# Performance work log

Measured on AMD Instinct MI355X. Metric: run time of the kernel, lower is better.

The kernel has to match this reference:

```python
import jax, jax.numpy as jnp
import numpy as np

D_MODEL = 1024
D_STATE = 8          # max(8, 16 // 2)
D_CONV = 4
D_INNER = int(1.5 * D_MODEL)   # expand = max(1.5, 2*0.75)
DT_RANK = (D_MODEL + 15) // 16 # 64
D_FF = 2 * D_MODEL
B, L = 2, 2048


def layer_norm(x, g, b, eps=1e-5):
    mu = jnp.mean(x, -1, keepdims=True)
    var = jnp.var(x, -1, keepdims=True)
    return (x - mu) * jax.lax.rsqrt(var + eps) * g + b


def setup_inputs() -> dict:
    key = jax.random.key(0)
    ks = jax.random.split(key, 12)
    def n(k, shape, scale=0.02):
        return jax.random.normal(k, shape, dtype=jnp.float32) * scale
    return {
        'x': jax.random.normal(ks[0], (B, L, D_MODEL), dtype=jnp.float32),
        'ln1_g': jnp.ones((D_MODEL,), jnp.float32),
        'ln1_b': jnp.zeros((D_MODEL,), jnp.float32),
        'ln2_g': jnp.ones((D_MODEL,), jnp.float32),
        'ln2_b': jnp.zeros((D_MODEL,), jnp.float32),
        'in_proj_w': n(ks[1], (2 * D_INNER, D_MODEL)),
        'conv_w': n(ks[2], (D_INNER, 1, D_CONV), 0.1),
        'conv_b': jnp.zeros((D_INNER,), jnp.float32),
        'x_proj_w': n(ks[3], (DT_RANK + 2 * D_STATE, D_INNER)),
        'dt_proj_w': n(ks[4], (D_INNER, DT_RANK), 0.1),
        'dt_proj_b': n(ks[5], (D_INNER,), 0.1),
        'A_log': jnp.log(jnp.broadcast_to(jnp.arange(1, D_STATE + 1, dtype=jnp.float32), (D_INNER, D_STATE))),
        'D': jnp.ones((D_INNER,), jnp.float32),
        'out_proj_w': n(ks[6], (D_MODEL, D_INNER)),
        'ffn_w1': n(ks[7], (D_FF, D_MODEL)),
        'ffn_b1': jnp.zeros((D_FF,), jnp.float32),
        'ffn_w2': n(ks[8], (D_MODEL, D_FF)),
        'ffn_b2': jnp.zeros((D_MODEL,), jnp.float32),
    }


def mamba(x, in_proj_w, conv_w, conv_b, x_proj_w, dt_proj_w, dt_proj_b, A_log, Dp, out_proj_w):
    # in_proj -> (x, z)
    xz = x @ in_proj_w.T                       # (B, L, 2*d_inner)
    xi, z = jnp.split(xz, 2, axis=-1)
    # depthwise causal conv over seq, kernel 4
    xc = jnp.transpose(xi, (0, 2, 1))          # (B, d_inner, L)
    xc = jax.lax.conv_general_dilated(
        xc, conv_w, window_strides=(1,), padding=[(D_CONV - 1, 0)],
        dimension_numbers=('NCH', 'OIH', 'NCH'), feature_group_count=D_INNER)
    xc = xc + conv_b[None, :, None]
    u = jax.nn.silu(jnp.transpose(xc, (0, 2, 1)))  # (B, L, d_inner)
    # x_proj -> dt, B, C
    x_dbl = u @ x_proj_w.T
    dt = x_dbl[..., :DT_RANK]
    Bm = x_dbl[..., DT_RANK:DT_RANK + D_STATE]
    Cm = x_dbl[..., DT_RANK + D_STATE:]
    delta = jax.nn.softplus(dt @ dt_proj_w.T + dt_proj_b)  # (B, L, d_inner)
    A = -jnp.exp(A_log)                                    # (d_inner, d_state)
    dA = jnp.exp(jnp.einsum('bld,dn->bldn', delta, A))     # (B, L, d_inner, d_state)
    dBu = jnp.einsum('bld,bln,bld->bldn', delta, Bm, u)
    # selective scan over time
    def step(h, inputs):
        dA_t, dBu_t, C_t = inputs
        h = dA_t * h + dBu_t                   # (B, d_inner, d_state)
        y = jnp.einsum('bdn,bn->bd', h, C_t)
        return h, y
    h0 = jnp.zeros((x.shape[0], D_INNER, D_STATE), x.dtype)
    _, ys = jax.lax.scan(step, h0, (jnp.moveaxis(dA, 1, 0), jnp.moveaxis(dBu, 1, 0), jnp.moveaxis(Cm, 1, 0)))
    y = jnp.moveaxis(ys, 0, 1) + u * Dp        # skip connection D*u
    y = y * jax.nn.silu(z)                     # gate
    return y @ out_proj_w.T


def reference(x, ln1_g, ln1_b, ln2_g, ln2_b, in_proj_w, conv_w, conv_b, x_proj_w,
              dt_proj_w, dt_proj_b, A_log, D, out_proj_w, ffn_w1, ffn_b1, ffn_w2, ffn_b2):
    residual = x
    xp = layer_norm(x, ln1_g, ln1_b)
    x = mamba(xp, in_proj_w, conv_w, conv_b, x_proj_w, dt_proj_w, dt_proj_b, A_log, D, out_proj_w) + residual
    xn = layer_norm(x, ln2_g, ln2_b)
    h = jax.nn.gelu(xn @ ffn_w1.T + ffn_b1, approximate=False)  # dropout is identity in eval
    return x + (h @ ffn_w2.T + ffn_b2)
```

## Files before the change

### kernel.cpp

```cpp
#include <hip/hip_runtime.h>
#include <math.h>

#define D_MODEL 1024
#define D_STATE 8
#define D_CONV  4
#define D_INNER 1536
#define DT_RANK 64
#define D_FF    2048
#define BATCH   2
#define SEQ     2048
#define NROWS   (BATCH*SEQ)
#define NC      32
#define LC      (SEQ/NC)
#define XPAD    128

typedef short bf16x8 __attribute__((ext_vector_type(8)));
typedef unsigned short u16x8 __attribute__((ext_vector_type(8)));
typedef float f32x4  __attribute__((ext_vector_type(4)));

__device__ inline unsigned short f2bf(float x) {
    union { float f; unsigned u; } v; v.f = x;
    unsigned r = v.u + 0x7fffu + ((v.u >> 16) & 1u);
    return (unsigned short)(r >> 16);
}
__device__ inline float bf2f(unsigned short h) {
    union { unsigned u; float f; } v; v.u = ((unsigned)h) << 16;
    return v.f;
}
__device__ inline float softplus_f(float x) {
    return (x > 20.0f) ? x : log1pf(__expf(x));
}
__device__ inline float gelu_f(float x) {
    return 0.5f * x * (1.0f + erff(x * 0.70710678118654752f));
}
__device__ inline float silu_f(float x) {
    return x / (1.0f + __expf(-x));
}
__device__ inline void gload16(const unsigned short* g, unsigned short* l) {
    typedef unsigned int u32;
    __builtin_amdgcn_global_load_lds(
        (const __attribute__((address_space(1))) u32*)g,
        (__attribute__((address_space(3))) u32*)l, 16, 0, 0);
}

#define PHASE_SYNC_PRE()  do { __builtin_amdgcn_s_barrier(); \
                               asm volatile("s_waitcnt lgkmcnt(0)" ::: "memory"); } while (0)
#define PHASE_SYNC_POST() do { __builtin_amdgcn_s_barrier(); } while (0)

__global__ __launch_bounds__(256) void prep_kernel(
    const float* __restrict__ s0, unsigned short* __restrict__ d0,
    const float* __restrict__ s1, unsigned short* __restrict__ d1,
    const float* __restrict__ s2, unsigned short* __restrict__ d2,
    const float* __restrict__ s3, unsigned short* __restrict__ d3,
    const float* __restrict__ s4, unsigned short* __restrict__ d4,
    const float* __restrict__ xpw, unsigned short* __restrict__ xpd,
    const float* __restrict__ x, const float* __restrict__ g1,
    const float* __restrict__ b1, unsigned short* __restrict__ xout) {
    int b = blockIdx.x;
    if (b < 4400) {
        const float* s; unsigned short* d; int base;
        if      (b < 1536) { s = s0; d = d0; base = b * 2048; }
        else if (b < 1584) { s = s1; d = d1; base = (b - 1536) * 2048; }
        else if (b < 2352) { s = s2; d = d2; base = (b - 1584) * 2048; }
        else if (b < 3376) { s = s3; d = d3; base = (b - 2352) * 2048; }
        else               { s = s4; d = d4; base = (b - 3376) * 2048; }
        int i = base + threadIdx.x * 8;
        float4 v0 = *(const float4*)(s + i);
        float4 v1 = *(const float4*)(s + i + 4);
        ushort4 a, c;
        a.x = f2bf(v0.x); a.y = f2bf(v0.y); a.z = f2bf(v0.z); a.w = f2bf(v0.w);
        c.x = f2bf(v1.x); c.y = f2bf(v1.y); c.z = f2bf(v1.z); c.w = f2bf(v1.w);
        *(ushort4*)(d + i)     = a;
        *(ushort4*)(d + i + 4) = c;
    } else if (b < 4528) {
        int row = b - 4400;
        for (int c = threadIdx.x; c < D_INNER; c += 256)
            xpd[row * D_INNER + c] = (row < 80) ? f2bf(xpw[row * D_INNER + c]) : (unsigned short)0;
    } else {
        __shared__ float sbuf[4];
        int row = b - 4528;
        int t = threadIdx.x;
        float4 v = ((const float4*)(x + (size_t)row * D_MODEL))[t];
        float s = v.x + v.y + v.z + v.w;
        for (int o = 32; o; o >>= 1) s += __shfl_down(s, o, 64);
        if ((t & 63) == 0) sbuf[t >> 6] = s;
        __syncthreads();
        float mu = (sbuf[0] + sbuf[1] + sbuf[2] + sbuf[3]) * (1.0f / D_MODEL);
        __syncthreads();
        float e0 = v.x - mu, e1 = v.y - mu, e2 = v.z - mu, e3 = v.w - mu;
        float q = e0*e0 + e1*e1 + e2*e2 + e3*e3;
        for (int o = 32; o; o >>= 1) q += __shfl_down(q, o, 64);
        if ((t & 63) == 0) sbuf[t >> 6] = q;
        __syncthreads();
        float var = (sbuf[0] + sbuf[1] + sbuf[2] + sbuf[3]) * (1.0f / D_MODEL);
        float rs = rsqrtf(var + 1e-5f);
        float4 gv = ((const float4*)g1)[t];
        float4 bv = ((const float4*)b1)[t];
        ushort4 st;
        st.x = f2bf(e0 * rs * gv.x + bv.x);
        st.y = f2bf(e1 * rs * gv.y + bv.y);
        st.z = f2bf(e2 * rs * gv.z + bv.z);
        st.w = f2bf(e3 * rs * gv.w + bv.w);
        ((ushort4*)(xout + (size_t)row * D_MODEL))[t] = st;
    }
}

#define EPI_F32        0
#define EPI_F32_BF16   1
#define EPI_SOFTPLUS   2
#define EPI_RESID      3
#define EPI_GELU_BF16  4
#define EPI_BIAS_RESID 5
#define EPI_BF16       6
#define EPI_SOFTPLUS_BF16 7
#define EPI_PBF16      9

template<int WN, int EPI, int SPLITK>
__global__ __launch_bounds__(512, 2) void gemm8p(
    const unsigned short* __restrict__ A, int lda,
    const unsigned short* __restrict__ Bm, int ldb, int K,
    float* __restrict__ Cf, unsigned short* __restrict__ Cb, int ldc,
    const float* __restrict__ bias,
    const float* __restrict__ resid, int ldr) {
    constexpr int WM = 8 / WN;
    constexpr int BN = WN * 64;
    constexpr int RW = 256 / WM;
    constexpr int CW = 64;
    constexpr int MI = RW / 16;
    constexpr int NI = CW / 16;
    constexpr int MIH = MI / 2, NIH = NI / 2;
    constexpr int ABYTES = 256 * 128;
    constexpr int BBYTES = BN * 128;
    constexpr int BOFF = 2 * ABYTES;
    __shared__ unsigned short lds[(2 * ABYTES + 2 * BBYTES) / 2];

    const int t = threadIdx.x, l = t & 63, w = t >> 6;
    const int wr = w / WN, wc = w % WN;

    const int nx = gridDim.x;
    const int nwg = nx * gridDim.y;
    int bid = blockIdx.y * nx + blockIdx.x;
    int q = nwg >> 3;
    int swz = (bid & 7) * q + (bid >> 3);
    const int m0 = (swz / nx) * 256, n0 = (swz % nx) * BN;
    const int kbase = (SPLITK > 1) ? blockIdx.z * K : 0;

    const int sr = l >> 3;
    const int sj = ((l & 7) * 16) ^ ((l >> 3) << 4);
    const int row_l = w * 8;
    const int row_c = (w >> 2) * 64 + (w & 3) * 8;

    auto STG = [&](int bufbyte, int rowbase, const unsigned short* G, int ldg, int gbase, int kt) {
        unsigned short* dst = (unsigned short*)((char*)lds + bufbyte + rowbase * 128);
        const unsigned short* src = G + (size_t)(gbase + rowbase + sr) * ldg + kbase + kt * 64 + (sj >> 1);
        gload16(src, dst);
    };
    auto S_Ah0 = [&](int b, int kt) {
        if (WN == 4) { STG(b * ABYTES, row_l, A, lda, m0, kt);       STG(b * ABYTES, 128 + row_l, A, lda, m0, kt); }
        else         { STG(b * ABYTES, row_c, A, lda, m0, kt);       STG(b * ABYTES, 128 + row_c, A, lda, m0, kt); }
    };
    auto S_Ah1 = [&](int b, int kt) {
        if (WN == 4) { STG(b * ABYTES, 64 + row_l, A, lda, m0, kt);  STG(b * ABYTES, 192 + row_l, A, lda, m0, kt); }
        else         { STG(b * ABYTES, 32 + row_c, A, lda, m0, kt);  STG(b * ABYTES, 160 + row_c, A, lda, m0, kt); }
    };
    auto S_Bc0 = [&](int b, int kt) {
        if (WN == 4) { STG(BOFF + b * BBYTES, row_c, Bm, ldb, n0, kt); STG(BOFF + b * BBYTES, 128 + row_c, Bm, ldb, n0, kt); }
        else         { STG(BOFF + b * BBYTES, row_c, Bm, ldb, n0, kt); }
    };
    auto S_Bc1 = [&](int b, int kt) {
        if (WN == 4) { STG(BOFF + b * BBYTES, 32 + row_c, Bm, ldb, n0, kt); STG(BOFF + b * BBYTES, 160 + row_c, Bm, ldb, n0, kt); }
        else         { STG(BOFF + b * BBYTES, 32 + row_c, Bm, ldb, n0, kt); }
    };

    auto LD = [&](int bytebase, int row, int kb) -> bf16x8 {
        int o = bytebase + row * 128 + (kb ^ ((row & 7) << 4));
        return *(const bf16x8*)((const char*)lds + o);
    };

    f32x4 acc[MI][NI] = {};
    bf16x8 af[MIH][2], b0v[NIH][2], b1v[NIH][2];

    auto LDA_set = [&](int buf, int qr, auto& dst) {
        #pragma unroll
        for (int mi = 0; mi < MIH; mi++)
            #pragma unroll
            for (int ks = 0; ks < 2; ks++)
                dst[mi][ks] = LD(buf * ABYTES, wr * RW + qr * (RW / 2) + mi * 16 + (l & 15),
                                 ks * 64 + (l >> 4) * 16);
    };
    auto LDB_set = [&](int buf, int qc, auto& dst) {
        #pragma unroll
        for (int ni2 = 0; ni2 < NIH; ni2++)
            #pragma unroll
            for (int ks = 0; ks < 2; ks++)
                dst[ni2][ks] = LD(BOFF + buf * BBYTES, wc * CW + qc * 32 + ni2 * 16 + (l & 15),
                                  ks * 64 + (l >> 4) * 16);
    };
    auto MFMA_Q = [&](int qr, int qc, auto& a_, auto& b_) {
        __builtin_amdgcn_s_setprio(1);
        #pragma unroll
        for (int mi = 0; mi < MIH; mi++)
            #pragma unroll
            for (int ni2 = 0; ni2 < NIH; ni2++)
                #pragma unroll
                for (int ks = 0; ks < 2; ks++)
                    acc[qr * MIH + mi][qc * NIH + ni2] =
                        __builtin_amdgcn_mfma_f32_16x16x32_bf16(a_[mi][ks], b_[ni2][ks],
                                                                acc[qr * MIH + mi][qc * NIH + ni2], 0, 0, 0);
        __builtin_amdgcn_s_setprio(0);
    };
    auto VMW = [&](bool last) {
        if (last)            asm volatile("s_waitcnt vmcnt(0)" ::: "memory");
        else if (WN == 4)    asm volatile("s_waitcnt vmcnt(6)" ::: "memory");
        else                 asm volatile("s_waitcnt vmcnt(5)" ::: "memory");
    };

    const int ni_ = K >> 7;

    S_Ah0(0, 0); S_Ah1(0, 0); S_Bc0(0, 0); S_Bc1(0, 0);
    S_Ah0(1, 1); S_Ah1(1, 1); S_Bc0(1, 1); S_Bc1(1, 1);
    if (WN == 4) asm volatile("s_waitcnt vmcnt(8)" ::: "memory");
    else         asm volatile("s_waitcnt vmcnt(6)" ::: "memory");
    __builtin_amdgcn_s_barrier();

    for (int i = 0; i < ni_; i++) {
        const bool last = (i == ni_ - 1);
        const int t2 = 2 * i + 2, t3 = 2 * i + 3;
        LDA_set(0, 0, af); LDB_set(0, 0, b0v);
        if (i) S_Bc0(1, 2 * i + 1);
        PHASE_SYNC_PRE(); MFMA_Q(0, 0, af, b0v); PHASE_SYNC_POST();
        LDB_set(0, 1, b1v);
        if (!last) S_Ah0(0, t2);
        PHASE_SYNC_PRE(); MFMA_Q(0, 1, af, b1v); PHASE_SYNC_POST();
        LDA_set(0, 1, af);
        PHASE_SYNC_PRE(); MFMA_Q(1, 1, af, b1v); PHASE_SYNC_POST();
        LDB_set(0, 0, b0v);
        if (!last) { S_Ah1(0, t2); S_Bc1(0, t2); }
        VMW(last);
        PHASE_SYNC_PRE(); MFMA_Q(1, 0, af, b0v); PHASE_SYNC_POST();
        LDA_set(1, 0, af); LDB_set(1, 0, b0v);
        if (!last) S_Bc0(0, t2);
        PHASE_SYNC_PRE(); MFMA_Q(0, 0, af, b0v); PHASE_SYNC_POST();
        LDB_set(1, 1, b1v);
        if (!last) S_Ah0(1, t3);
        PHASE_SYNC_PRE(); MFMA_Q(0, 1, af, b1v); PHASE_SYNC_POST();
        LDA_set(1, 1, af);
        PHASE_SYNC_PRE(); MFMA_Q(1, 1, af, b1v); PHASE_SYNC_POST();
        LDB_set(1, 0, b0v);
        if (!last) { S_Ah1(1, t3); S_Bc1(1, t3); }
        VMW(last);
        PHASE_SYNC_PRE(); MFMA_Q(1, 0, af, b0v); PHASE_SYNC_POST();
    }

    float* Cfp = Cf;
    unsigned short* Cbp = Cb;
    if (SPLITK > 1) {
        Cfp += (size_t)blockIdx.z * NROWS * ldc;
        Cbp += (size_t)blockIdx.z * NROWS * ldc;
    }
    #pragma unroll
    for (int ni2 = 0; ni2 < NI; ni2++) {
        int col = n0 + wc * CW + ni2 * 16 + (l & 15);
        float bv = 0.0f;
        if (EPI == EPI_SOFTPLUS || EPI == EPI_GELU_BF16 || EPI == EPI_BIAS_RESID) bv = bias[col];
        #pragma unroll
        for (int mi = 0; mi < MI; mi++) {
            #pragma unroll
            for (int j = 0; j < 4; j++) {
                int row = m0 + wr * RW + mi * 16 + (l >> 4) * 4 + j;
                float v = acc[mi][ni2][j];
                if (EPI == EPI_SOFTPLUS)        v = softplus_f(v + bv);
                else if (EPI == EPI_GELU_BF16)  v = gelu_f(v + bv);
                else if (EPI == EPI_RESID)      v = v + resid[(size_t)row * ldr + col];
                else if (EPI == EPI_BIAS_RESID) v = v + bv + resid[(size_t)row * ldr + col];
                if (EPI == EPI_GELU_BF16 || EPI == EPI_BF16 || EPI == EPI_PBF16) {
                    Cbp[(size_t)row * ldc + col] = f2bf(v);
                } else {
                    Cfp[(size_t)row * ldc + col] = v;
                    if (EPI == EPI_F32_BF16) Cbp[(size_t)row * ldc + col] = f2bf(v);
                }
            }
        }
    }
}

__global__ __launch_bounds__(256) void sk2_ln(const unsigned short* __restrict__ p,
                                              const float* __restrict__ resid,
                                              const float* __restrict__ g,
                                              const float* __restrict__ b,
                                              float* __restrict__ x2,
                                              unsigned short* __restrict__ xn) {
    __shared__ float sbuf[4];
    int row = blockIdx.x;
    int t = threadIdx.x;
    const size_t seg = (size_t)NROWS * D_MODEL;
    size_t base = (size_t)row * D_MODEL + t * 4;
    ushort4 a = *(const ushort4*)(p + base);
    ushort4 bb = *(const ushort4*)(p + base + seg);
    float4 r = *(const float4*)(resid + base);
    float4 v;
    v.x = bf2f(a.x) + bf2f(bb.x) + r.x;
    v.y = bf2f(a.y) + bf2f(bb.y) + r.y;
    v.z = bf2f(a.z) + bf2f(bb.z) + r.z;
    v.w = bf2f(a.w) + bf2f(bb.w) + r.w;
    *(float4*)(x2 + base) = v;
    float s = v.x + v.y + v.z + v.w;
    for (int o = 32; o; o >>= 1) s += __shfl_down(s, o, 64);
    if ((t & 63) == 0) sbuf[t >> 6] = s;
    __syncthreads();
    float mu = (sbuf[0] + sbuf[1] + sbuf[2] + sbuf[3]) * (1.0f / D_MODEL);
    __syncthreads();
    float d0 = v.x - mu, d1 = v.y - mu, d2 = v.z - mu, d3 = v.w - mu;
    float qq = d0*d0 + d1*d1 + d2*d2 + d3*d3;
    for (int o = 32; o; o >>= 1) qq += __shfl_down(qq, o, 64);
    if ((t & 63) == 0) sbuf[t >> 6] = qq;
    __syncthreads();
    float var = (sbuf[0] + sbuf[1] + sbuf[2] + sbuf[3]) * (1.0f / D_MODEL);
    float rs = rsqrtf(var + 1e-5f);
    float4 gv = ((const float4*)g)[t];
    float4 bv = ((const float4*)b)[t];
    ushort4 st;
    st.x = f2bf(d0 * rs * gv.x + bv.x);
    st.y = f2bf(d1 * rs * gv.y + bv.y);
    st.z = f2bf(d2 * rs * gv.z + bv.z);
    st.w = f2bf(d3 * rs * gv.w + bv.w);
    ((ushort4*)(xn + (size_t)row * D_MODEL))[t] = st;
}

__global__ __launch_bounds__(256) void sk2_reduce(const unsigned short* __restrict__ p,
                                                  const float* __restrict__ bias,
                                                  const float* __restrict__ resid,
                                                  float* __restrict__ o) {
    int i = (blockIdx.x * 256 + threadIdx.x) * 4;
    const size_t seg = (size_t)NROWS * D_MODEL;
    ushort4 a = *(const ushort4*)(p + i);
    ushort4 b = *(const ushort4*)(p + i + seg);
    float4 r = *(const float4*)(resid + i);
    float4 bb = *(const float4*)(bias + (i & (D_MODEL - 1)));
    float4 o4;
    o4.x = bf2f(a.x) + bf2f(b.x) + r.x + bb.x;
    o4.y = bf2f(a.y) + bf2f(b.y) + r.y + bb.y;
    o4.z = bf2f(a.z) + bf2f(b.z) + r.z + bb.z;
    o4.w = bf2f(a.w) + bf2f(b.w) + r.w + bb.w;
    *(float4*)(o + i) = o4;
}

template<int EPI, int SPLITK>
__global__ __launch_bounds__(256) void gemm_mfma(
    const unsigned short* __restrict__ A, int lda,
    const unsigned short* __restrict__ B, int ldb, int K,
    float* __restrict__ Cf, unsigned short* __restrict__ Cb, int ldc,
    const float* __restrict__ bias,
    const float* __restrict__ resid, int ldr) {
    __shared__ unsigned short As[3][128 * 32];
    __shared__ unsigned short Bs[3][128 * 32];
    int t = threadIdx.x, l = t & 63, w = t >> 6;
    int nx = gridDim.x;
    int nwg = nx * gridDim.y;
    int bid = blockIdx.y * nx + blockIdx.x;
    int q = nwg >> 3;
    int swz = (bid & 7) * q + (bid >> 3);
    int m0 = (swz / nx) * 128, n0 = (swz % nx) * 128;
    int kbase = (SPLITK > 1) ? blockIdx.z * K : 0;
    int c0 = 2 * w, c1 = 2 * w + 1;
    int srow = l >> 2, scol = (l & 3) * 8;
    const unsigned short* Ag0 = A + (size_t)(m0 + 16 * c0 + srow) * lda + kbase + scol;
    const unsigned short* Ag1 = A + (size_t)(m0 + 16 * c1 + srow) * lda + kbase + scol;
    const unsigned short* Bg0 = B + (size_t)(n0 + 16 * c0 + srow) * ldb + kbase + scol;
    const unsigned short* Bg1 = B + (size_t)(n0 + 16 * c1 + srow) * ldb + kbase + scol;
    int wr = w >> 1, wc = w & 1;
    int aoff = (wr * 64 + (l & 15)) * 32 + (l >> 4) * 8;
    int boff = (wc * 64 + (l & 15)) * 32 + (l >> 4) * 8;

    f32x4 acc[4][4] = {};
    int nt = K >> 5;

    gload16(Ag0, &As[0][c0 * 512]);
    gload16(Ag1, &As[0][c1 * 512]);
    gload16(Bg0, &Bs[0][c0 * 512]);
    gload16(Bg1, &Bs[0][c1 * 512]);
    if (nt > 1) {
        gload16(Ag0 + 32, &As[1][c0 * 512]);
        gload16(Ag1 + 32, &As[1][c1 * 512]);
        gload16(Bg0 + 32, &Bs[1][c0 * 512]);
        gload16(Bg1 + 32, &Bs[1][c1 * 512]);
    }

    int cur = 0;
    for (int ti = 0; ti < nt; ti++) {
        int pf = ti + 2;
        if (pf < nt) {
            int nb = cur - 1; if (nb < 0) nb += 3;
            int k0 = pf << 5;
            gload16(Ag0 + k0, &As[nb][c0 * 512]);
            gload16(Ag1 + k0, &As[nb][c1 * 512]);
            gload16(Bg0 + k0, &Bs[nb][c0 * 512]);
            gload16(Bg1 + k0, &Bs[nb][c1 * 512]);
        }
        int rem = nt - 1 - ti;
        if (rem >= 2)      asm volatile("s_waitcnt vmcnt(8)" ::: "memory");
        else if (rem == 1) asm volatile("s_waitcnt vmcnt(4)" ::: "memory");
        else               asm volatile("s_waitcnt vmcnt(0)" ::: "memory");
        __builtin_amdgcn_s_barrier();

        const unsigned short* Ab = &As[cur][0];
        const unsigned short* Bb = &Bs[cur][0];
        bf16x8 af[4], bfv[4];
        #pragma unroll
        for (int i = 0; i < 4; i++) af[i] = *(const bf16x8*)(Ab + aoff + i * 512);
        #pragma unroll
        for (int i = 0; i < 4; i++) bfv[i] = *(const bf16x8*)(Bb + boff + i * 512);
        __builtin_amdgcn_s_setprio(1);
        #pragma unroll
        for (int mi = 0; mi < 4; mi++)
            #pragma unroll
            for (int ni = 0; ni < 4; ni++)
                acc[mi][ni] = __builtin_amdgcn_mfma_f32_16x16x32_bf16(af[mi], bfv[ni], acc[mi][ni], 0, 0, 0);
        __builtin_amdgcn_s_setprio(0);
        __builtin_amdgcn_s_barrier();
        cur++; if (cur == 3) cur = 0;
    }

    if (SPLITK > 1) Cf += (size_t)blockIdx.z * NROWS * ldc;
    int colb = n0 + wc * 64 + (l & 15);
    int rowb = m0 + wr * 64 + (l >> 4) * 4;
    #pragma unroll
    for (int ni = 0; ni < 4; ni++) {
        int col = colb + ni * 16;
        float bv = 0.0f;
        if (EPI == EPI_SOFTPLUS_BF16) bv = bias[col];
        #pragma unroll
        for (int mi = 0; mi < 4; mi++) {
            #pragma unroll
            for (int j = 0; j < 4; j++) {
                int row = rowb + mi * 16 + j;
                float v = acc[mi][ni][j];
                if (EPI == EPI_SOFTPLUS_BF16) v = softplus_f(v + bv);
                if (EPI == EPI_BF16 || EPI == EPI_SOFTPLUS_BF16) {
                    Cb[(size_t)row * ldc + col] = f2bf(v);
                } else {
                    Cf[(size_t)row * ldc + col] = v;
                }
            }
        }
    }
}

__global__ __launch_bounds__(256) void xdbl_reduce(const float* __restrict__ part,
                                                   float* __restrict__ xdbl,
                                                   unsigned short* __restrict__ xdbl_bf) {
    int i = blockIdx.x * 256 + threadIdx.x;
    const size_t seg = (size_t)NROWS * XPAD;
    float s = part[i] + part[i + seg] + part[i + 2 * seg] + part[i + 3 * seg];
    xdbl[i] = s;
    xdbl_bf[i] = f2bf(s);
}

__global__ __launch_bounds__(256) void conv_silu(const unsigned short* __restrict__ xz,
                                                 const float* __restrict__ w,
                                                 const float* __restrict__ cb,
                                                 unsigned short* __restrict__ u) {
    int idx = (blockIdx.x * 256 + threadIdx.x) * 8;
    int d = idx % D_INNER;
    int bl = idx / D_INNER;
    int l = bl & (SEQ - 1);
    float acc[8];
    float4 wv[8];
    #pragma unroll
    for (int j = 0; j < 8; j++) wv[j] = *(const float4*)(w + (d + j) * 4);
    float4 cb0 = *(const float4*)(cb + d);
    float4 cb1 = *(const float4*)(cb + d + 4);
    acc[0] = cb0.x; acc[1] = cb0.y; acc[2] = cb0.z; acc[3] = cb0.w;
    acc[4] = cb1.x; acc[5] = cb1.y; acc[6] = cb1.z; acc[7] = cb1.w;
    #pragma unroll
    for (int k = 0; k < 4; k++) {
        int lp = l - 3 + k;
        if (lp >= 0) {
            u16x8 s = *(const u16x8*)(xz + (size_t)(bl - 3 + k) * (2 * D_INNER) + d);
            #pragma unroll
            for (int j = 0; j < 8; j++) {
                float wk = (k == 0) ? wv[j].x : (k == 1) ? wv[j].y : (k == 2) ? wv[j].z : wv[j].w;
                acc[j] += bf2f((unsigned short)s[j]) * wk;
            }
        }
    }
    u16x8 o;
    #pragma unroll
    for (int j = 0; j < 8; j++) o[j] = f2bf(silu_f(acc[j]));
    *(u16x8*)(u + idx) = o;
}

__global__ __launch_bounds__(256) void scan_passA(const unsigned short* __restrict__ delta,
                                                  const unsigned short* __restrict__ u,
                                                  const float* __restrict__ xdbl,
                                                  const float* __restrict__ A_log,
                                                  float* __restrict__ P,
                                                  float* __restrict__ S) {
    int d = blockIdx.x * 256 + threadIdx.x;
    int c = blockIdx.y, b = blockIdx.z;
    __shared__ float bc[LC][16];
    int base_row = b * SEQ + c * LC;
    for (int e = threadIdx.x; e < LC * 16; e += 256) {
        int lrr = e >> 4, col = e & 15;
        bc[lrr][col] = xdbl[(size_t)(base_row + lrr) * XPAD + DT_RANK + col];
    }
    __syncthreads();
    float Ad[8];
    #pragma unroll
    for (int n = 0; n < 8; n++) Ad[n] = -__expf(A_log[d * 8 + n]);
    float prod[8], hs[8];
    #pragma unroll
    for (int n = 0; n < 8; n++) { prod[n] = 1.0f; hs[n] = 0.0f; }
    for (int lrr = 0; lrr < LC; lrr++) {
        int row = base_row + lrr;
        float dl = bf2f(delta[(size_t)row * D_INNER + d]);
        float uu = bf2f(u[(size_t)row * D_INNER + d]);
        float du = dl * uu;
        #pragma unroll
        for (int n = 0; n < 8; n++) {
            float dA = __expf(dl * Ad[n]);
            prod[n] *= dA;
            hs[n] = dA * hs[n] + du * bc[lrr][n];
        }
    }
    size_t o = ((size_t)((size_t)b * NC + c) * D_INNER + d) * 8;
    #pragma unroll
    for (int n = 0; n < 8; n++) { P[o + n] = prod[n]; S[o + n] = hs[n]; }
}

__global__ __launch_bounds__(256) void scan_passB(const float* __restrict__ P,
                                                  const float* __restrict__ S,
                                                  float* __restrict__ hstart) {
    int tid = blockIdx.x * 256 + threadIdx.x;
    int b = tid / (D_INNER * 8);
    int rem = tid % (D_INNER * 8);
    float h = 0.0f;
    for (int c = 0; c < NC; c++) {
        size_t o = (size_t)(b * NC + c) * (D_INNER * 8) + rem;
        hstart[o] = h;
        h = P[o] * h + S[o];
    }
}

__global__ __launch_bounds__(256) void scan_passC(const unsigned short* __restrict__ delta,
                                                  const unsigned short* __restrict__ u,
                                                  const float* __restrict__ xdbl,
                                                  const float* __restrict__ A_log,
                                                  const float* __restrict__ hstart,
                                                  const unsigned short* __restrict__ xz,
                                                  const float* __restrict__ Dp,
                                                  unsigned short* __restrict__ ygate) {
    int d = blockIdx.x * 256 + threadIdx.x;
    int c = blockIdx.y, b = blockIdx.z;
    __shared__ float bc[LC][16];
    int base_row = b * SEQ + c * LC;
    for (int e = threadIdx.x; e < LC * 16; e += 256) {
        int lrr = e >> 4, col = e & 15;
        bc[lrr][col] = xdbl[(size_t)(base_row + lrr) * XPAD + DT_RANK + col];
    }
    __syncthreads();
    float Ad[8];
    #pragma unroll
    for (int n = 0; n < 8; n++) Ad[n] = -__expf(A_log[d * 8 + n]);
    float h[8];
    size_t ho = ((size_t)((size_t)b * NC + c) * D_INNER + d) * 8;
    #pragma unroll
    for (int n = 0; n < 8; n++) h[n] = hstart[ho + n];
    float Dd = Dp[d];
    for (int lrr = 0; lrr < LC; lrr++) {
        int row = base_row + lrr;
        float dl = bf2f(delta[(size_t)row * D_INNER + d]);
        float uu = bf2f(u[(size_t)row * D_INNER + d]);
        float du = dl * uu;
        float y = 0.0f;
        #pragma unroll
        for (int n = 0; n < 8; n++) {
            float dA = __expf(dl * Ad[n]);
            h[n] = dA * h[n] + du * bc[lrr][n];
            y += h[n] * bc[lrr][8 + n];
        }
        y += uu * Dd;
        float z = bf2f(xz[(size_t)row * (2 * D_INNER) + D_INNER + d]);
        ygate[(size_t)row * D_INNER + d] = f2bf(y * silu_f(z));
    }
}

extern "C" void kernel_launch(void* const* d_in, const int* in_sizes, int n_in,
                              void* d_out, int out_size, void* d_ws, size_t ws_size,
                              hipStream_t stream) {
    const float* x         = (const float*)d_in[0];
    const float* ln1_g     = (const float*)d_in[1];
    const float* ln1_b     = (const float*)d_in[2];
    const float* ln2_g     = (const float*)d_in[3];
    const float* ln2_b     = (const float*)d_in[4];
    const float* in_proj_w = (const float*)d_in[5];
    const float* conv_w    = (const float*)d_in[6];
    const float* conv_b    = (const float*)d_in[7];
    const float* x_proj_w  = (const float*)d_in[8];
    const float* dt_proj_w = (const float*)d_in[9];
    const float* dt_proj_b = (const float*)d_in[10];
    const float* A_log     = (const float*)d_in[11];
    const float* Dp        = (const float*)d_in[12];
    const float* out_proj_w= (const float*)d_in[13];
    const float* ffn_w1    = (const float*)d_in[14];
    const float* ffn_b1    = (const float*)d_in[15];
    const float* ffn_w2    = (const float*)d_in[16];
    const float* ffn_b2    = (const float*)d_in[17];
    float* out = (float*)d_out;

    float* xdbl  = (float*)d_ws;
    float* P     = xdbl + (size_t)NROWS * XPAD;
    float* S     = P + (size_t)BATCH * NC * D_INNER * 8;
    float* hst   = S + (size_t)BATCH * NC * D_INNER * 8;
    float* x2    = hst + (size_t)BATCH * NC * D_INNER * 8;
    float* part  = x2 + (size_t)NROWS * D_MODEL;
    unsigned short* psum_bf = (unsigned short*)(part + 4 * (size_t)NROWS * XPAD);
    unsigned short* xz_bf   = psum_bf + 2 * (size_t)NROWS * D_MODEL;
    unsigned short* xp_bf   = xz_bf + (size_t)NROWS * 2 * D_INNER;
    unsigned short* u_bf    = xp_bf + (size_t)NROWS * D_MODEL;
    unsigned short* xdbl_bf = u_bf + (size_t)NROWS * D_INNER;
    unsigned short* yg_bf   = xdbl_bf + (size_t)NROWS * XPAD;
    unsigned short* dl_bf   = yg_bf + (size_t)NROWS * D_INNER;
    unsigned short* w_in    = dl_bf + (size_t)NROWS * D_INNER;
    unsigned short* w_xp    = w_in + (size_t)2 * D_INNER * D_MODEL;
    unsigned short* w_dt    = w_xp + (size_t)XPAD * D_INNER;
    unsigned short* w_out   = w_dt + (size_t)D_INNER * DT_RANK;
    unsigned short* w_f1    = w_out + (size_t)D_MODEL * D_INNER;
    unsigned short* w_f2    = w_f1 + (size_t)D_FF * D_MODEL;
    unsigned short* hff_bf  = xz_bf;

    prep_kernel<<<4400 + XPAD + NROWS, 256, 0, stream>>>(
        in_proj_w, w_in, dt_proj_w, w_dt, out_proj_w, w_out, ffn_w1, w_f1, ffn_w2, w_f2,
        x_proj_w, w_xp, x, ln1_g, ln1_b, xp_bf);
    gemm8p<4, EPI_BF16, 1><<<dim3(3072 / 256, NROWS / 256), 512, 0, stream>>>(
        xp_bf, D_MODEL, w_in, D_MODEL, D_MODEL, nullptr, xz_bf, 2 * D_INNER, nullptr, nullptr, 0);
    conv_silu<<<(NROWS * D_INNER) / (256 * 8), 256, 0, stream>>>(xz_bf, conv_w, conv_b, u_bf);
    gemm_mfma<EPI_F32, 4><<<dim3(1, NROWS / 128, 4), 256, 0, stream>>>(
        u_bf, D_INNER, w_xp, D_INNER, D_INNER / 4, part, nullptr, XPAD, nullptr, nullptr, 0);
    xdbl_reduce<<<(NROWS * XPAD) / 256, 256, 0, stream>>>(part, xdbl, xdbl_bf);
    gemm_mfma<EPI_SOFTPLUS_BF16, 1><<<dim3(D_INNER / 128, NROWS / 128), 256, 0, stream>>>(
        xdbl_bf, XPAD, w_dt, DT_RANK, DT_RANK, nullptr, dl_bf, D_INNER, dt_proj_b, nullptr, 0);
    scan_passA<<<dim3(D_INNER / 256, NC, BATCH), 256, 0, stream>>>(dl_bf, u_bf, xdbl, A_log, P, S);
    scan_passB<<<(BATCH * D_INNER * 8) / 256, 256, 0, stream>>>(P, S, hst);
    scan_passC<<<dim3(D_INNER / 256, NC, BATCH), 256, 0, stream>>>(dl_bf, u_bf, xdbl, A_log, hst, xz_bf, Dp, yg_bf);
    gemm8p<2, EPI_PBF16, 2><<<dim3(D_MODEL / 128, NROWS / 256, 2), 512, 0, stream>>>(
        yg_bf, D_INNER, w_out, D_INNER, D_INNER / 2, nullptr, psum_bf, D_MODEL, nullptr, nullptr, 0);
    sk2_ln<<<NROWS, 256, 0, stream>>>(psum_bf, x, ln2_g, ln2_b, x2, xp_bf);
    gemm8p<2, EPI_GELU_BF16, 1><<<dim3(D_FF / 128, NROWS / 256), 512, 0, stream>>>(
        xp_bf, D_MODEL, w_f1, D_MODEL, D_MODEL, nullptr, hff_bf, D_FF, ffn_b1, nullptr, 0);
    gemm8p<2, EPI_PBF16, 2><<<dim3(D_MODEL / 128, NROWS / 256, 2), 512, 0, stream>>>(
        hff_bf, D_FF, w_f2, D_FF, D_FF / 2, nullptr, psum_bf, D_MODEL, nullptr, nullptr, 0);
    sk2_reduce<<<(NROWS * D_MODEL) / 1024, 256, 0, stream>>>(psum_bf, ffn_b2, x2, out);
}
```

Measured before the change: 276.0 us.

## Fuse depthwise conv+SiLU into split-K x_proj GEMM and fold reduction into dt_proj

Removes the standalone conv_silu kernel by computing the causal conv and SiLU while staging A tiles inside a new x_proj GEMM kernel, which also writes u. The split-K partials are stored as bf16 in a 512-wide buffer. The separate reduce kernel is eliminated by replicating the dt_proj weight four times along K, so the dt GEMM sums the partials implicitly, and the scan kernels sum the four B/C partials on load. This cuts two launches and intermediate fp32 traffic, but makes the dt GEMM four times longer in K and drops B/C precision to bf16 partial sums.

```diff
diff --git a/kernel.cpp b/kernel.cpp
--- a/kernel.cpp
+++ b/kernel.cpp
@@ -12,7 +12,7 @@
 #define NROWS   (BATCH*SEQ)
 #define NC      32
 #define LC      (SEQ/NC)
-#define XPAD    128
+#define XQW     512
 
 typedef short bf16x8 __attribute__((ext_vector_type(8)));
 typedef unsigned short u16x8 __attribute__((ext_vector_type(8)));
@@ -57,13 +57,12 @@
     const float* __restrict__ x, const float* __restrict__ g1,
     const float* __restrict__ b1, unsigned short* __restrict__ xout) {
     int b = blockIdx.x;
-    if (b < 4400) {
+    if (b < 1536 || (b >= 1920 && b < 4736)) {
         const float* s; unsigned short* d; int base;
         if      (b < 1536) { s = s0; d = d0; base = b * 2048; }
-        else if (b < 1584) { s = s1; d = d1; base = (b - 1536) * 2048; }
-        else if (b < 2352) { s = s2; d = d2; base = (b - 1584) * 2048; }
-        else if (b < 3376) { s = s3; d = d3; base = (b - 2352) * 2048; }
-        else               { s = s4; d = d4; base = (b - 3376) * 2048; }
+        else if (b < 2688) { s = s2; d = d2; base = (b - 1920) * 2048; }
+        else if (b < 3712) { s = s3; d = d3; base = (b - 2688) * 2048; }
+        else               { s = s4; d = d4; base = (b - 3712) * 2048; }
         int i = base + threadIdx.x * 8;
         float4 v0 = *(const float4*)(s + i);
         float4 v1 = *(const float4*)(s + i + 4);
@@ -72,13 +71,24 @@
         c.x = f2bf(v1.x); c.y = f2bf(v1.y); c.z = f2bf(v1.z); c.w = f2bf(v1.w);
         *(ushort4*)(d + i)     = a;
         *(ushort4*)(d + i + 4) = c;
-    } else if (b < 4528) {
-        int row = b - 4400;
+    } else if (b < 1920) {
+        int i = (b - 1536) * 2048 + threadIdx.x * 8;
+        int r = i >> 9;
+        int j = i & 511;
+        u16x8 o;
+        #pragma unroll
+        for (int jj = 0; jj < 8; jj++) {
+            int c = (j + jj) & 127;
+            o[jj] = (c < 64) ? f2bf(s1[r * 64 + c]) : (unsigned short)0;
+        }
+        *(u16x8*)(d1 + i) = o;
+    } else if (b < 4864) {
+        int row = b - 4736;
         for (int c = threadIdx.x; c < D_INNER; c += 256)
             xpd[row * D_INNER + c] = (row < 80) ? f2bf(xpw[row * D_INNER + c]) : (unsigned short)0;
     } else {
         __shared__ float sbuf[4];
-        int row = b - 4528;
+        int row = b - 4864;
         int t = threadIdx.x;
         float4 v = ((const float4*)(x + (size_t)row * D_MODEL))[t];
         float s = v.x + v.y + v.z + v.w;
@@ -106,11 +116,7 @@
 }
 
 #define EPI_F32        0
-#define EPI_F32_BF16   1
-#define EPI_SOFTPLUS   2
-#define EPI_RESID      3
 #define EPI_GELU_BF16  4
-#define EPI_BIAS_RESID 5
 #define EPI_BF16       6
 #define EPI_SOFTPLUS_BF16 7
 #define EPI_PBF16      9
@@ -262,22 +268,18 @@
     for (int ni2 = 0; ni2 < NI; ni2++) {
         int col = n0 + wc * CW + ni2 * 16 + (l & 15);
         float bv = 0.0f;
-        if (EPI == EPI_SOFTPLUS || EPI == EPI_GELU_BF16 || EPI == EPI_BIAS_RESID) bv = bias[col];
+        if (EPI == EPI_GELU_BF16) bv = bias[col];
         #pragma unroll
         for (int mi = 0; mi < MI; mi++) {
             #pragma unroll
             for (int j = 0; j < 4; j++) {
                 int row = m0 + wr * RW + mi * 16 + (l >> 4) * 4 + j;
                 float v = acc[mi][ni2][j];
-                if (EPI == EPI_SOFTPLUS)        v = softplus_f(v + bv);
-                else if (EPI == EPI_GELU_BF16)  v = gelu_f(v + bv);
-                else if (EPI == EPI_RESID)      v = v + resid[(size_t)row * ldr + col];
-                else if (EPI == EPI_BIAS_RESID) v = v + bv + resid[(size_t)row * ldr + col];
+                if (EPI == EPI_GELU_BF16)  v = gelu_f(v + bv);
                 if (EPI == EPI_GELU_BF16 || EPI == EPI_BF16 || EPI == EPI_PBF16) {
                     Cbp[(size_t)row * ldc + col] = f2bf(v);
                 } else {
                     Cfp[(size_t)row * ldc + col] = v;
-                    if (EPI == EPI_F32_BF16) Cbp[(size_t)row * ldc + col] = f2bf(v);
                 }
             }
         }
@@ -345,13 +347,102 @@
     *(float4*)(o + i) = o4;
 }
 
-template<int EPI, int SPLITK>
+__global__ __launch_bounds__(256) void xproj_conv_gemm(
+    const unsigned short* __restrict__ xz, const float* __restrict__ cw,
+    const float* __restrict__ cb, unsigned short* __restrict__ u,
+    const unsigned short* __restrict__ B,
+    unsigned short* __restrict__ xq) {
+    __shared__ unsigned short As[128 * 32];
+    __shared__ unsigned short Bs[128 * 32];
+    int t = threadIdx.x, l = t & 63, w = t >> 6;
+    int m0 = blockIdx.x * 128;
+    int kbase = blockIdx.y * 384;
+    int c0 = 2 * w, c1 = 2 * w + 1;
+    int srow = l >> 2, scol = (l & 3) * 8;
+    const unsigned short* Bg0 = B + (size_t)(16 * c0 + srow) * D_INNER + kbase + scol;
+    const unsigned short* Bg1 = B + (size_t)(16 * c1 + srow) * D_INNER + kbase + scol;
+    int wr = w >> 1, wc = w & 1;
+    int aoff = (wr * 64 + (l & 15)) * 32 + (l >> 4) * 8;
+    int boff = (wc * 64 + (l & 15)) * 32 + (l >> 4) * 8;
+
+    f32x4 acc[4][4] = {};
+
+    for (int ti = 0; ti < 12; ti++) {
+        int k0 = ti * 32;
+        gload16(Bg0 + k0, &Bs[c0 * 512]);
+        gload16(Bg1 + k0, &Bs[c1 * 512]);
+        #pragma unroll
+        for (int cc = 0; cc < 2; cc++) {
+            int ch = 2 * w + cc;
+            int bl = m0 + 16 * ch + srow;
+            int d0 = kbase + k0 + scol;
+            int lq = bl & (SEQ - 1);
+            u16x8 rr[4];
+            #pragma unroll
+            for (int kk = 0; kk < 4; kk++) {
+                if (lq - 3 + kk >= 0)
+                    rr[kk] = *(const u16x8*)(xz + (size_t)(bl - 3 + kk) * (2 * D_INNER) + d0);
+                else
+                    rr[kk] = (u16x8)0;
+            }
+            float4 cb0 = *(const float4*)(cb + d0);
+            float4 cb1 = *(const float4*)(cb + d0 + 4);
+            float av[8];
+            av[0] = cb0.x; av[1] = cb0.y; av[2] = cb0.z; av[3] = cb0.w;
+            av[4] = cb1.x; av[5] = cb1.y; av[6] = cb1.z; av[7] = cb1.w;
+            u16x8 o;
+            #pragma unroll
+            for (int j = 0; j < 8; j++) {
+                float4 wv = *(const float4*)(cw + (d0 + j) * 4);
+                float s = av[j];
+                s += bf2f((unsigned short)rr[0][j]) * wv.x;
+                s += bf2f((unsigned short)rr[1][j]) * wv.y;
+                s += bf2f((unsigned short)rr[2][j]) * wv.z;
+                s += bf2f((unsigned short)rr[3][j]) * wv.w;
+                o[j] = f2bf(silu_f(s));
+            }
+            *(u16x8*)(&As[ch * 512 + l * 8]) = o;
+            *(u16x8*)(u + (size_t)bl * D_INNER + d0) = o;
+        }
+        __syncthreads();
+        bf16x8 af[4], bfv[4];
+        #pragma unroll
+        for (int i = 0; i < 4; i++) af[i] = *(const bf16x8*)(&As[aoff + i * 512]);
+        #pragma unroll
+        for (int i = 0; i < 4; i++) bfv[i] = *(const bf16x8*)(&Bs[boff + i * 512]);
+        __builtin_amdgcn_s_setprio(1);
+        #pragma unroll
+        for (int mi = 0; mi < 4; mi++)
+            #pragma unroll
+            for (int ni = 0; ni < 4; ni++)
+                acc[mi][ni] = __builtin_amdgcn_mfma_f32_16x16x32_bf16(af[mi], bfv[ni], acc[mi][ni], 0, 0, 0);
+        __builtin_amdgcn_s_setprio(0);
+        __syncthreads();
+    }
+
+    unsigned short* Cb = xq + blockIdx.y * 128;
+    int colb = wc * 64 + (l & 15);
+    int rowb = m0 + wr * 64 + (l >> 4) * 4;
+    #pragma unroll
+    for (int ni = 0; ni < 4; ni++) {
+        int col = colb + ni * 16;
+        #pragma unroll
+        for (int mi = 0; mi < 4; mi++) {
+            #pragma unroll
+            for (int j = 0; j < 4; j++) {
+                int row = rowb + mi * 16 + j;
+                Cb[(size_t)row * XQW + col] = f2bf(acc[mi][ni][j]);
+            }
+        }
+    }
+}
+
+template<int EPI>
 __global__ __launch_bounds__(256) void gemm_mfma(
     const unsigned short* __restrict__ A, int lda,
     const unsigned short* __restrict__ B, int ldb, int K,
     float* __restrict__ Cf, unsigned short* __restrict__ Cb, int ldc,
-    const float* __restrict__ bias,
-    const float* __restrict__ resid, int ldr) {
+    const float* __restrict__ bias) {
     __shared__ unsigned short As[3][128 * 32];
     __shared__ unsigned short Bs[3][128 * 32];
     int t = threadIdx.x, l = t & 63, w = t >> 6;
@@ -361,13 +452,12 @@
     int q = nwg >> 3;
     int swz = (bid & 7) * q + (bid >> 3);
     int m0 = (swz / nx) * 128, n0 = (swz % nx) * 128;
-    int kbase = (SPLITK > 1) ? blockIdx.z * K : 0;
     int c0 = 2 * w, c1 = 2 * w + 1;
     int srow = l >> 2, scol = (l & 3) * 8;
-    const unsigned short* Ag0 = A + (size_t)(m0 + 16 * c0 + srow) * lda + kbase + scol;
-    const unsigned short* Ag1 = A + (size_t)(m0 + 16 * c1 + srow) * lda + kbase + scol;
-    const unsigned short* Bg0 = B + (size_t)(n0 + 16 * c0 + srow) * ldb + kbase + scol;
-    const unsigned short* Bg1 = B + (size_t)(n0 + 16 * c1 + srow) * ldb + kbase + scol;
+    const unsigned short* Ag0 = A + (size_t)(m0 + 16 * c0 + srow) * lda + scol;
+    const unsigned short* Ag1 = A + (size_t)(m0 + 16 * c1 + srow) * lda + scol;
+    const unsigned short* Bg0 = B + (size_t)(n0 + 16 * c0 + srow) * ldb + scol;
+    const unsigned short* Bg1 = B + (size_t)(n0 + 16 * c1 + srow) * ldb + scol;
     int wr = w >> 1, wc = w & 1;
     int aoff = (wr * 64 + (l & 15)) * 32 + (l >> 4) * 8;
     int boff = (wc * 64 + (l & 15)) * 32 + (l >> 4) * 8;
@@ -421,7 +511,6 @@
         cur++; if (cur == 3) cur = 0;
     }
 
-    if (SPLITK > 1) Cf += (size_t)blockIdx.z * NROWS * ldc;
     int colb = n0 + wc * 64 + (l & 15);
     int rowb = m0 + wr * 64 + (l >> 4) * 4;
     #pragma unroll
@@ -446,53 +535,9 @@
     }
 }
 
-__global__ __launch_bounds__(256) void xdbl_reduce(const float* __restrict__ part,
-                                                   float* __restrict__ xdbl,
-                                                   unsigned short* __restrict__ xdbl_bf) {
-    int i = blockIdx.x * 256 + threadIdx.x;
-    const size_t seg = (size_t)NROWS * XPAD;
-    float s = part[i] + part[i + seg] + part[i + 2 * seg] + part[i + 3 * seg];
-    xdbl[i] = s;
-    xdbl_bf[i] = f2bf(s);
-}
-
-__global__ __launch_bounds__(256) void conv_silu(const unsigned short* __restrict__ xz,
-                                                 const float* __restrict__ w,
-                                                 const float* __restrict__ cb,
-                                                 unsigned short* __restrict__ u) {
-    int idx = (blockIdx.x * 256 + threadIdx.x) * 8;
-    int d = idx % D_INNER;
-    int bl = idx / D_INNER;
-    int l = bl & (SEQ - 1);
-    float acc[8];
-    float4 wv[8];
-    #pragma unroll
-    for (int j = 0; j < 8; j++) wv[j] = *(const float4*)(w + (d + j) * 4);
-    float4 cb0 = *(const float4*)(cb + d);
-    float4 cb1 = *(const float4*)(cb + d + 4);
-    acc[0] = cb0.x; acc[1] = cb0.y; acc[2] = cb0.z; acc[3] = cb0.w;
-    acc[4] = cb1.x; acc[5] = cb1.y; acc[6] = cb1.z; acc[7] = cb1.w;
-    #pragma unroll
-    for (int k = 0; k < 4; k++) {
-        int lp = l - 3 + k;
-        if (lp >= 0) {
-            u16x8 s = *(const u16x8*)(xz + (size_t)(bl - 3 + k) * (2 * D_INNER) + d);
-            #pragma unroll
-            for (int j = 0; j < 8; j++) {
-                float wk = (k == 0) ? wv[j].x : (k == 1) ? wv[j].y : (k == 2) ? wv[j].z : wv[j].w;
-                acc[j] += bf2f((unsigned short)s[j]) * wk;
-            }
-        }
-    }
-    u16x8 o;
-    #pragma unroll
-    for (int j = 0; j < 8; j++) o[j] = f2bf(silu_f(acc[j]));
-    *(u16x8*)(u + idx) = o;
-}
-
 __global__ __launch_bounds__(256) void scan_passA(const unsigned short* __restrict__ delta,
                                                   const unsigned short* __restrict__ u,
-                                                  const float* __restrict__ xdbl,
+                                                  const unsigned short* __restrict__ xq,
                                                   const float* __restrict__ A_log,
                                                   float* __restrict__ P,
                                                   float* __restrict__ S) {
@@ -502,7 +547,8 @@
     int base_row = b * SEQ + c * LC;
     for (int e = threadIdx.x; e < LC * 16; e += 256) {
         int lrr = e >> 4, col = e & 15;
-        bc[lrr][col] = xdbl[(size_t)(base_row + lrr) * XPAD + DT_RANK + col];
+        const unsigned short* xr = xq + (size_t)(base_row + lrr) * XQW + 64 + col;
+        bc[lrr][col] = bf2f(xr[0]) + bf2f(xr[128]) + bf2f(xr[256]) + bf2f(xr[384]);
     }
     __syncthreads();
     float Ad[8];
@@ -544,7 +590,7 @@
 
 __global__ __launch_bounds__(256) void scan_passC(const unsigned short* __restrict__ delta,
                                                   const unsigned short* __restrict__ u,
-                                                  const float* __restrict__ xdbl,
+                                                  const unsigned short* __restrict__ xq,
                                                   const float* __restrict__ A_log,
                                                   const float* __restrict__ hstart,
                                                   const unsigned short* __restrict__ xz,
@@ -556,7 +602,8 @@
     int base_row = b * SEQ + c * LC;
     for (int e = threadIdx.x; e < LC * 16; e += 256) {
         int lrr = e >> 4, col = e & 15;
-        bc[lrr][col] = xdbl[(size_t)(base_row + lrr) * XPAD + DT_RANK + col];
+        const unsigned short* xr = xq + (size_t)(base_row + lrr) * XQW + 64 + col;
+        bc[lrr][col] = bf2f(xr[0]) + bf2f(xr[128]) + bf2f(xr[256]) + bf2f(xr[384]);
     }
     __syncthreads();
     float Ad[8];
@@ -608,41 +655,37 @@
     const float* ffn_b2    = (const float*)d_in[17];
     float* out = (float*)d_out;
 
-    float* xdbl  = (float*)d_ws;
-    float* P     = xdbl + (size_t)NROWS * XPAD;
+    float* P     = (float*)d_ws;
     float* S     = P + (size_t)BATCH * NC * D_INNER * 8;
     float* hst   = S + (size_t)BATCH * NC * D_INNER * 8;
     float* x2    = hst + (size_t)BATCH * NC * D_INNER * 8;
-    float* part  = x2 + (size_t)NROWS * D_MODEL;
-    unsigned short* psum_bf = (unsigned short*)(part + 4 * (size_t)NROWS * XPAD);
-    unsigned short* xz_bf   = psum_bf + 2 * (size_t)NROWS * D_MODEL;
+    unsigned short* psum_bf = (unsigned short*)(x2 + (size_t)NROWS * D_MODEL);
+    unsigned short* xq      = psum_bf + 2 * (size_t)NROWS * D_MODEL;
+    unsigned short* xz_bf   = xq + (size_t)NROWS * XQW;
     unsigned short* xp_bf   = xz_bf + (size_t)NROWS * 2 * D_INNER;
     unsigned short* u_bf    = xp_bf + (size_t)NROWS * D_MODEL;
-    unsigned short* xdbl_bf = u_bf + (size_t)NROWS * D_INNER;
-    unsigned short* yg_bf   = xdbl_bf + (size_t)NROWS * XPAD;
+    unsigned short* yg_bf   = u_bf + (size_t)NROWS * D_INNER;
     unsigned short* dl_bf   = yg_bf + (size_t)NROWS * D_INNER;
     unsigned short* w_in    = dl_bf + (size_t)NROWS * D_INNER;
     unsigned short* w_xp    = w_in + (size_t)2 * D_INNER * D_MODEL;
-    unsigned short* w_dt    = w_xp + (size_t)XPAD * D_INNER;
-    unsigned short* w_out   = w_dt + (size_t)D_INNER * DT_RANK;
+    unsigned short* w_dt4   = w_xp + (size_t)128 * D_INNER;
+    unsigned short* w_out   = w_dt4 + (size_t)D_INNER * XQW;
     unsigned short* w_f1    = w_out + (size_t)D_MODEL * D_INNER;
     unsigned short* w_f2    = w_f1 + (size_t)D_FF * D_MODEL;
     unsigned short* hff_bf  = xz_bf;
 
-    prep_kernel<<<4400 + XPAD + NROWS, 256, 0, stream>>>(
-        in_proj_w, w_in, dt_proj_w, w_dt, out_proj_w, w_out, ffn_w1, w_f1, ffn_w2, w_f2,
+    prep_kernel<<<8960, 256, 0, stream>>>(
+        in_proj_w, w_in, dt_proj_w, w_dt4, out_proj_w, w_out, ffn_w1, w_f1, ffn_w2, w_f2,
         x_proj_w, w_xp, x, ln1_g, ln1_b, xp_bf);
     gemm8p<4, EPI_BF16, 1><<<dim3(3072 / 256, NROWS / 256), 512, 0, stream>>>(
         xp_bf, D_MODEL, w_in, D_MODEL, D_MODEL, nullptr, xz_bf, 2 * D_INNER, nullptr, nullptr, 0);
-    conv_silu<<<(NROWS * D_INNER) / (256 * 8), 256, 0, stream>>>(xz_bf, conv_w, conv_b, u_bf);
-    gemm_mfma<EPI_F32, 4><<<dim3(1, NROWS / 128, 4), 256, 0, stream>>>(
-        u_bf, D_INNER, w_xp, D_INNER, D_INNER / 4, part, nullptr, XPAD, nullptr, nullptr, 0);
-    xdbl_reduce<<<(NROWS * XPAD) / 256, 256, 0, stream>>>(part, xdbl, xdbl_bf);
-    gemm_mfma<EPI_SOFTPLUS_BF16, 1><<<dim3(D_INNER / 128, NROWS / 128), 256, 0, stream>>>(
-        xdbl_bf, XPAD, w_dt, DT_RANK, DT_RANK, nullptr, dl_bf, D_INNER, dt_proj_b, nullptr, 0);
-    scan_passA<<<dim3(D_INNER / 256, NC, BATCH), 256, 0, stream>>>(dl_bf, u_bf, xdbl, A_log, P, S);
+    xproj_conv_gemm<<<dim3(NROWS / 128, 4), 256, 0, stream>>>(
+        xz_bf, conv_w, conv_b, u_bf, w_xp, xq);
+    gemm_mfma<EPI_SOFTPLUS_BF16><<<dim3(D_INNER / 128, NROWS / 128), 256, 0, stream>>>(
+        xq, XQW, w_dt4, XQW, XQW, nullptr, dl_bf, D_INNER, dt_proj_b);
+    scan_passA<<<dim3(D_INNER / 256, NC, BATCH), 256, 0, stream>>>(dl_bf, u_bf, xq, A_log, P, S);
     scan_passB<<<(BATCH * D_INNER * 8) / 256, 256, 0, stream>>>(P, S, hst);
-    scan_passC<<<dim3(D_INNER / 256, NC, BATCH), 256, 0, stream>>>(dl_bf, u_bf, xdbl, A_log, hst, xz_bf, Dp, yg_bf);
+    scan_passC<<<dim3(D_INNER / 256, NC, BATCH), 256, 0, stream>>>(dl_bf, u_bf, xq, A_log, hst, xz_bf, Dp, yg_bf);
     gemm8p<2, EPI_PBF16, 2><<<dim3(D_MODEL / 128, NROWS / 256, 2), 512, 0, stream>>>(
         yg_bf, D_INNER, w_out, D_INNER, D_INNER / 2, nullptr, psum_bf, D_MODEL, nullptr, nullptr, 0);
     sk2_ln<<<NROWS, 256, 0, stream>>>(psum_bf, x, ln2_g, ln2_b, x2, xp_bf);
```

Result: no change. 274.1 us (-0.7%).
